# Performance work log

Measured on AMD Instinct MI355X. Metric: run time of the kernel, lower is better.

The kernel has to match this reference:

```python
import jax, jax.numpy as jnp
import numpy as np

B_, L_, D_ = 2, 1024, 512   # batch, seq_len, dim
H_ = 8                      # num_heads, head_dim = 64
Q_ = 64                     # chunk size for the chunked semi-separable scan


def setup_inputs() -> dict:
    key = jax.random.key(0)
    ks = jax.random.split(key, 7)
    s = 1.0 / np.sqrt(D_)   # torch nn.Linear default init bound
    x = jax.random.normal(ks[0], (B_, L_, D_), dtype=jnp.float32)
    W_A = jax.random.uniform(ks[1], (D_, D_), jnp.float32, -s, s)
    b_A = jax.random.uniform(ks[2], (D_,), jnp.float32, -s, s)
    W_B = jax.random.uniform(ks[3], (D_, D_), jnp.float32, -s, s)
    b_B = jax.random.uniform(ks[4], (D_,), jnp.float32, -s, s)
    W_C = jax.random.uniform(ks[5], (D_, D_), jnp.float32, -s, s)
    b_C = jax.random.uniform(ks[6], (D_,), jnp.float32, -s, s)
    return {"x": x, "W_A": W_A, "b_A": b_A, "W_B": W_B, "b_B": b_B,
            "W_C": W_C, "b_C": b_C}


def _semi_separable_T(x, W_A, b_A, W_B, b_B, W_C, b_C):
    """T_ij = sum_d C_{i,d} * (prod_{k=j+1}^{i-1} A_{k,d}) * B_{j,d}, j <= i.

    Computed in log space with Mamba2-style chunking: all exponent
    differences are <= 0, so exp() underflows to 0 (the true limit)
    instead of producing inf/nan as a naive cumprod-quotient would.
    """
    B, L, D = x.shape
    H = H_
    Dh = D // H
    Q = Q_
    nc = L // Q
    NEG = -jnp.inf

    A = jax.nn.sigmoid(x @ W_A.T + b_A)    # [B,L,D], values in (0,1)
    Bf = x @ W_B.T + b_B
    C = x @ W_C.T + b_C

    def heads(t):
        return t.reshape(B, L, H, Dh).transpose(0, 2, 1, 3)  # [B,H,L,Dh]

    A, Bf, C = heads(A), heads(Bf), heads(C)

    S = jnp.cumsum(jnp.log(A), axis=2)                       # S[k] = sum_{0..k} log A
    Sm1 = jnp.concatenate([jnp.zeros_like(S[:, :, :1]), S[:, :, :-1]], axis=2)
    # prod_{k=j+1}^{i-1} A_k = exp(Sm1[i] - S[j])  for i >= j+1 (==1 at i=j+1)

    def chunk(t):
        return t.reshape(B, H, nc, Q, Dh)

    Sc, Sm1c, Bc, Cc = chunk(S), chunk(Sm1), chunk(Bf), chunk(C)

    qi = jnp.arange(Q)[:, None]
    ki = jnp.arange(Q)[None, :]
    lower = (qi > ki)[None, None, None, :, :, None]
    diag = (qi == ki)[None, None, None, :, :, None]

    # ---- diagonal blocks (within-chunk, strictly lower + diagonal) ----
    diff = Sm1c[:, :, :, :, None, :] - Sc[:, :, :, None, :, :]  # [B,H,nc,Q,Q,Dh], <=0 where q>k
    dec = jnp.where(lower, diff, jnp.where(diag, 0.0, NEG))     # q==k -> prod=1
    Tdiag = jnp.einsum('bhmqd,bhmqkd,bhmkd->bhmqk', Cc, jnp.exp(dec), Bc)

    # ---- cross blocks (chunk m queries vs chunk n<m keys) ----
    E = Sc[:, :, :, -1, :]                                      # S at last index of each chunk
    Eprev = jnp.concatenate([jnp.zeros_like(E[:, :, :1]), E[:, :, :-1]], axis=2)
    qf = Cc * jnp.exp(Sm1c - Eprev[:, :, :, None, :])           # exponent <= 0
    kf = Bc * jnp.exp(E[:, :, :, None, :] - Sc)                 # exponent <= 0
    mi = jnp.arange(nc)[:, None]
    ni = jnp.arange(nc)[None, :]
    cross_mask = (ni < mi)[None, None, :, :, None]
    Dcross = jnp.exp(jnp.where(cross_mask,
                               Eprev[:, :, :, None, :] - E[:, :, None, :, :],
                               NEG))                            # [B,H,nc,nc,Dh]
    T = jnp.einsum('bhmqd,bhmnd,bhnkd->bhmqnk', qf, Dcross, kf)

    idx = jnp.arange(nc)
    T = T.at[:, :, idx, :, idx, :].set(jnp.moveaxis(Tdiag, 2, 0))
    return T.reshape(B, H, L, L)


def reference(x, W_A, b_A, W_B, b_B, W_C, b_C):
    return _semi_separable_T(x, W_A, b_A, W_B, b_B, W_C, b_C)
```

## Files before the change

### kernel.cpp

```cpp
#include <hip/hip_runtime.h>
#include <math.h>

#define BB 2
#define LL 1024
#define DD 512
#define HH 8
#define DHD 64
#define QQ 64
#define NCC 16

typedef __attribute__((ext_vector_type(8))) short s8b;
typedef __attribute__((ext_vector_type(4))) float f4;

__device__ __forceinline__ void bf16split(float f, unsigned short& h, unsigned short& l) {
    unsigned u  = __float_as_uint(f);
    unsigned hb = (u + 0x7FFFu + ((u >> 16) & 1u)) & 0xFFFF0000u;
    float fh = __uint_as_float(hb);
    float fl = f - fh;
    unsigned ul = __float_as_uint(fl);
    unsigned lb = (ul + 0x7FFFu + ((ul >> 16) & 1u)) >> 16;
    h = (unsigned short)(hb >> 16);
    l = (unsigned short)lb;
}

__device__ __forceinline__ unsigned pk2(unsigned short a, unsigned short b) {
    return (unsigned)a | ((unsigned)b << 16);
}

__global__ __launch_bounds__(512) void gemm3_fused(
    const float* __restrict__ x,
    const float* __restrict__ Wa, const float* __restrict__ ba,
    const float* __restrict__ Wb, const float* __restrict__ bb,
    const float* __restrict__ Wc, const float* __restrict__ bc,
    float* __restrict__ logA, float* __restrict__ Bf, float* __restrict__ Cf,
    float* __restrict__ csum)
{
    __shared__ unsigned char lds[65536];
    __shared__ float csv[64];

    const int bm = blockIdx.x >> 3;
    const int bn = blockIdx.x & 7;
    const int m0 = bm << 6, o0 = bn << 6;
    const int t = threadIdx.x, wv = t >> 6, ln = t & 63;
    const int l15 = ln & 15, l4 = ln >> 4;
    const int wr = (wv >> 2) << 5;
    const int wc = (wv & 3) << 4;

    const int src_id = wv >> 1;
    const float* srcp =
        (src_id == 0) ? x + (size_t)m0 * DD :
        ((src_id == 1) ? Wa : (src_id == 2) ? Wb : Wc) + (size_t)o0 * DD;
    const int roff = ((wv & 1) << 5) + (ln >> 1);
    const int ksh  = (ln & 1) << 4;
    const int swz  = (roff >> 1) & 3;
    const int sA   = ((ksh >> 3) + 0) ^ swz;
    const int sB   = ((ksh >> 3) + 1) ^ swz;
    const size_t srow = (size_t)roff * DD + ksh;
    const int hiBase = (src_id * 2) * 4096 + roff * 64;

    f4 acc[3][2] = {};

    auto STAGE = [&](int buf, int kt) {
        const float* p = srcp + srow + kt;
        const float4 f0 = *(const float4*)(p + 0);
        const float4 f1 = *(const float4*)(p + 4);
        const float4 f2 = *(const float4*)(p + 8);
        const float4 f3 = *(const float4*)(p + 12);
        const float v[16] = {f0.x,f0.y,f0.z,f0.w, f1.x,f1.y,f1.z,f1.w,
                             f2.x,f2.y,f2.z,f2.w, f3.x,f3.y,f3.z,f3.w};
        unsigned short h[16], l[16];
        #pragma unroll
        for (int i = 0; i < 16; ++i) bf16split(v[i], h[i], l[i]);
        unsigned char* bh = lds + buf * 32768 + hiBase;
        unsigned char* bl = bh + 4096;
        *(uint4*)(bh + sA * 16) = make_uint4(pk2(h[0],h[1]),  pk2(h[2],h[3]),
                                             pk2(h[4],h[5]),  pk2(h[6],h[7]));
        *(uint4*)(bh + sB * 16) = make_uint4(pk2(h[8],h[9]),  pk2(h[10],h[11]),
                                             pk2(h[12],h[13]),pk2(h[14],h[15]));
        *(uint4*)(bl + sA * 16) = make_uint4(pk2(l[0],l[1]),  pk2(l[2],l[3]),
                                             pk2(l[4],l[5]),  pk2(l[6],l[7]));
        *(uint4*)(bl + sB * 16) = make_uint4(pk2(l[8],l[9]),  pk2(l[10],l[11]),
                                             pk2(l[12],l[13]),pk2(l[14],l[15]));
    };

    auto ldso = [&](int row, int kg) {
        return row * 64 + ((kg ^ ((row >> 1) & 3)) << 4);
    };

    auto COMPUTE = [&](int buf) {
        const unsigned char* base = lds + buf * 32768;
        const s8b ah0 = *(const s8b*)(base + 0*4096 + ldso(wr      + l15, l4));
        const s8b ah1 = *(const s8b*)(base + 0*4096 + ldso(wr + 16 + l15, l4));
        const s8b al0 = *(const s8b*)(base + 1*4096 + ldso(wr      + l15, l4));
        const s8b al1 = *(const s8b*)(base + 1*4096 + ldso(wr + 16 + l15, l4));
        #pragma unroll
        for (int s = 0; s < 3; ++s) {
            const s8b bh = *(const s8b*)(base + (2 + 2*s)*4096 + ldso(wc + l15, l4));
            const s8b bl = *(const s8b*)(base + (3 + 2*s)*4096 + ldso(wc + l15, l4));
            acc[s][0] = __builtin_amdgcn_mfma_f32_16x16x32_bf16(ah0, bh, acc[s][0], 0, 0, 0);
            acc[s][1] = __builtin_amdgcn_mfma_f32_16x16x32_bf16(ah1, bh, acc[s][1], 0, 0, 0);
            acc[s][0] = __builtin_amdgcn_mfma_f32_16x16x32_bf16(ah0, bl, acc[s][0], 0, 0, 0);
            acc[s][1] = __builtin_amdgcn_mfma_f32_16x16x32_bf16(ah1, bl, acc[s][1], 0, 0, 0);
            acc[s][0] = __builtin_amdgcn_mfma_f32_16x16x32_bf16(al0, bh, acc[s][0], 0, 0, 0);
            acc[s][1] = __builtin_amdgcn_mfma_f32_16x16x32_bf16(al1, bh, acc[s][1], 0, 0, 0);
        }
    };

    STAGE(0, 0);
    __syncthreads();
    int cur = 0;
    for (int it = 0; it < 16; ++it) {
        if (it < 15) STAGE(cur ^ 1, (it + 1) * 32);
        COMPUTE(cur);
        __syncthreads();
        cur ^= 1;
    }

    const int col = o0 + wc + l15;
    const float bva = ba[col], bvb = bb[col], bvc = bc[col];
    float asum = 0.f;
    #pragma unroll
    for (int ms = 0; ms < 2; ++ms) {
        const int row0 = m0 + wr + ms * 16 + l4 * 4;
        #pragma unroll
        for (int r = 0; r < 4; ++r) {
            const size_t o = (size_t)(row0 + r) * DD + col;
            float va = acc[0][ms][r] + bva;
            va = fminf(va, 0.f) - log1pf(__expf(-fabsf(va)));
            logA[o] = va;
            asum += va;
            Bf[o] = acc[1][ms][r] + bvb;
            Cf[o] = acc[2][ms][r] + bvc;
        }
    }

    asum += __shfl_xor(asum, 16);
    asum += __shfl_xor(asum, 32);
    if (wv < 4 && l4 == 0) csv[wc + l15] = asum;
    __syncthreads();
    if (wv >= 4 && l4 == 0) {
        const int blkc = (((bm >> 4) * 8 + bn) << 4) + (bm & 15);
        csum[(size_t)blkc * DHD + wc + l15] = csv[wc + l15] + asum;
    }
}

__global__ __launch_bounds__(256) void scan_diag(
    const float* __restrict__ logA, const float* __restrict__ Bf,
    const float* __restrict__ Cf, const float* __restrict__ csum,
    float* __restrict__ qf, float* __restrict__ kf,
    float* __restrict__ coff, float* __restrict__ out)
{
    __shared__ float part[4][DHD];
    __shared__ float smA[DHD][65];
    __shared__ float smB[DHD][65];
    __shared__ float smC[DHD][65];

    const int blk = blockIdx.x;
    const int bh = blk >> 4, c = blk & 15;
    const int b = bh >> 3, h = bh & 7;
    const int t = threadIdx.x;
    const int d = t & 63, w = t >> 6;

    const size_t gbase = (size_t)(b * LL + c * QQ + w * 16) * DD + h * DHD + d;
    float lar[16];
    float ps = 0.f;
    #pragma unroll
    for (int i = 0; i < 16; ++i) {
        lar[i] = logA[gbase + (size_t)i * DD];
        ps += lar[i];
    }
    part[w][d] = ps;
    __syncthreads();

    const size_t cs0 = ((size_t)bh << 4) * DHD + d;
    float off = 0.f;
    for (int cc = 0; cc < c; ++cc) off += csum[cs0 + (size_t)cc * DHD];
    const float tot = part[0][d] + part[1][d] + part[2][d] + part[3][d];
    if (t < DHD) {
        coff[((size_t)bh * 17 + c) * DHD + t] = off;
        if (c == NCC - 1) coff[((size_t)bh * 17 + 16) * DHD + t] = off + tot;
    }

    float run = 0.f;
    for (int ww = 0; ww < 4; ++ww) if (ww < w) run += part[ww][d];

    const size_t hbase = ((size_t)bh * LL + c * QQ + w * 16) * DHD + d;
    #pragma unroll
    for (int i = 0; i < 16; ++i) {
        const size_t gi = gbase + (size_t)i * DD;
        const float cv = Cf[gi];
        const float bv = Bf[gi];
        qf[hbase + (size_t)i * DHD] = cv * __expf(run);
        run += lar[i];
        const int rloc = w * 16 + i;
        smC[d][rloc] = run;
        smA[d][rloc] = cv;
        smB[d][rloc] = bv;
        kf[hbase + (size_t)i * DHD] = bv * __expf(tot - run);
    }
    __syncthreads();

    const int q0 = ((t >> 4) & 15) << 2;
    const int k0 = (t & 15) << 2;

    float acc[4][4] = {};
    if (q0 + 3 >= k0) {
        #pragma unroll 2
        for (int dd = 0; dd < DHD; ++dd) {
            const float4 cq = *(const float4*)&smA[dd][q0];
            const float4 bk = *(const float4*)&smB[dd][k0];
            const float4 sk = *(const float4*)&smC[dd][k0];
            const float cqa[4] = {cq.x, cq.y, cq.z, cq.w};
            const float bka[4] = {bk.x, bk.y, bk.z, bk.w};
            const float ska[4] = {sk.x, sk.y, sk.z, sk.w};
            float s1a[4];
            #pragma unroll
            for (int i = 0; i < 4; ++i) {
                const int qi = q0 + i;
                s1a[i] = (qi == 0) ? 0.f : smC[dd][qi - 1];
            }
            #pragma unroll
            for (int i = 0; i < 4; ++i) {
                #pragma unroll
                for (int j = 0; j < 4; ++j) {
                    const int qi = q0 + i, kj = k0 + j;
                    const float wgt = (qi > kj) ? __expf(s1a[i] - ska[j])
                                                : ((qi == kj) ? 1.f : 0.f);
                    acc[i][j] += cqa[i] * wgt * bka[j];
                }
            }
        }
    }
    const size_t outrow0 = ((size_t)bh * LL + (size_t)c * QQ) * LL + (size_t)c * QQ;
    #pragma unroll
    for (int i = 0; i < 4; ++i)
        *(float4*)&out[outrow0 + (size_t)(q0 + i) * LL + k0] =
            make_float4(acc[i][0], acc[i][1], acc[i][2], acc[i][3]);

    for (int z = blk; z < BB * HH * 120; z += 256) {
        const int zbh = z / 120;
        const int idx = z - zbh * 120;
        int a = (int)((1.0f + sqrtf(1.0f + 8.0f * (float)idx)) * 0.5f);
        if (a * (a - 1) / 2 > idx) --a;
        else if ((a + 1) * a / 2 <= idx) ++a;
        const int zm = idx - a * (a - 1) / 2;
        const int zn = a;
        const size_t zb = ((size_t)zbh * LL + (size_t)zm * QQ) * LL + (size_t)zn * QQ;
        const float4 zz = make_float4(0.f, 0.f, 0.f, 0.f);
        #pragma unroll
        for (int r = 0; r < 4; ++r) {
            const int fi = t + (r << 8);
            const int row = fi >> 4;
            const int col = (fi & 15) << 2;
            *(float4*)&out[zb + (size_t)row * LL + col] = zz;
        }
    }
}

__global__ __launch_bounds__(256) void band_row(
    const float* __restrict__ qf, const float* __restrict__ kf,
    const float* __restrict__ coff, float* __restrict__ out)
{
    __shared__ unsigned char lds[49152];
    unsigned char* const l_qh = lds;
    unsigned char* const l_ql = lds + 8192;

    const int raw  = blockIdx.x;
    const int xcd  = raw & 7;
    const int kk   = raw >> 3;
    const int bh   = ((kk & 1) << 3) | xcd;
    const int rem  = kk >> 1;
    const int m    = rem >> 2;
    const int q4   = rem & 3;
    const int n0   = q4 << 2;

    const int t  = threadIdx.x;
    const int wv = t >> 6;
    const int ln = t & 63;
    const int l15 = ln & 15;
    const int l4  = ln >> 4;
    const int wr = (wv >> 1) << 5;
    const int wc = (wv & 1) << 5;

    const int srow = t >> 2;
    const int skc  = (t & 3) << 4;
    const int slot0 = skc >> 3;

    const size_t cb = (size_t)bh * 17 * DHD;
    const size_t outbase = ((size_t)bh * LL + (size_t)m * QQ) * LL;

    const int ne = (m < n0 + 4) ? m : (n0 + 4);
    if (n0 >= ne) return;

    float cm[16];
    #pragma unroll
    for (int g = 0; g < 4; ++g) {
        const float4 a = *(const float4*)&coff[cb + (size_t)m * DHD + skc + g * 4];
        cm[g*4+0]=a.x; cm[g*4+1]=a.y; cm[g*4+2]=a.z; cm[g*4+3]=a.w;
    }

    {
        const size_t qb = ((size_t)bh * LL + (size_t)m * QQ + srow) * DHD + skc;
        float v[16];
        #pragma unroll
        for (int g = 0; g < 4; ++g) {
            const float4 x4 = *(const float4*)&qf[qb + g * 4];
            v[g*4+0]=x4.x; v[g*4+1]=x4.y; v[g*4+2]=x4.z; v[g*4+3]=x4.w;
        }
        unsigned short h[16], l[16];
        #pragma unroll
        for (int i = 0; i < 16; ++i) bf16split(v[i], h[i], l[i]);
        *(uint4*)(l_qh + slot0*1024 + srow*16) =
            make_uint4(pk2(h[0],h[1]), pk2(h[2],h[3]), pk2(h[4],h[5]), pk2(h[6],h[7]));
        *(uint4*)(l_qh + (slot0+1)*1024 + srow*16) =
            make_uint4(pk2(h[8],h[9]), pk2(h[10],h[11]), pk2(h[12],h[13]), pk2(h[14],h[15]));
        *(uint4*)(l_ql + slot0*1024 + srow*16) =
            make_uint4(pk2(l[0],l[1]), pk2(l[2],l[3]), pk2(l[4],l[5]), pk2(l[6],l[7]));
        *(uint4*)(l_ql + (slot0+1)*1024 + srow*16) =
            make_uint4(pk2(l[8],l[9]), pk2(l[10],l[11]), pk2(l[12],l[13]), pk2(l[14],l[15]));
    }

    auto LOAD_K = [&](int n, float* vk, float* vc) {
        const size_t kb = ((size_t)bh * LL + (size_t)n * QQ + srow) * DHD + skc;
        #pragma unroll
        for (int g = 0; g < 4; ++g) {
            const float4 x4 = *(const float4*)&kf[kb + g * 4];
            vk[g*4+0]=x4.x; vk[g*4+1]=x4.y; vk[g*4+2]=x4.z; vk[g*4+3]=x4.w;
            const float4 c4 = *(const float4*)&coff[cb + (size_t)(n + 1) * DHD + skc + g * 4];
            vc[g*4+0]=c4.x; vc[g*4+1]=c4.y; vc[g*4+2]=c4.z; vc[g*4+3]=c4.w;
        }
    };

    auto WRITE_K = [&](int buf, const float* vk, const float* vc) {
        unsigned char* const kh_b = lds + 16384 + buf * 16384;
        unsigned char* const kl_b = kh_b + 8192;
        float v[16];
        #pragma unroll
        for (int i = 0; i < 16; ++i)
            v[i] = vk[i] * __expf(cm[i] - vc[i]);
        unsigned short h[16], l[16];
        #pragma unroll
        for (int i = 0; i < 16; ++i) bf16split(v[i], h[i], l[i]);
        *(uint4*)(kh_b + slot0*1024 + srow*16) =
            make_uint4(pk2(h[0],h[1]), pk2(h[2],h[3]), pk2(h[4],h[5]), pk2(h[6],h[7]));
        *(uint4*)(kh_b + (slot0+1)*1024 + srow*16) =
            make_uint4(pk2(h[8],h[9]), pk2(h[10],h[11]), pk2(h[12],h[13]), pk2(h[14],h[15]));
        *(uint4*)(kl_b + slot0*1024 + srow*16) =
            make_uint4(pk2(l[0],l[1]), pk2(l[2],l[3]), pk2(l[4],l[5]), pk2(l[6],l[7]));
        *(uint4*)(kl_b + (slot0+1)*1024 + srow*16) =
            make_uint4(pk2(l[8],l[9]), pk2(l[10],l[11]), pk2(l[12],l[13]), pk2(l[14],l[15]));
    };

    {
        float pk0[16], pc0[16];
        LOAD_K(n0, pk0, pc0);
        WRITE_K(0, pk0, pc0);
    }
    __syncthreads();

    int cur = 0;
    for (int n = n0; n < ne; ++n) {
        float nk[16], nc[16];
        const bool pre = (n + 1 < ne);
        if (pre) LOAD_K(n + 1, nk, nc);

        const unsigned char* const kh_b = lds + 16384 + cur * 16384;
        const unsigned char* const kl_b = kh_b + 8192;

        f4 acc[2][2] = {};
        #pragma unroll
        for (int ks = 0; ks < 2; ++ks) {
            const int ka = (ks * 4 + l4) * 1024;
            const s8b kh0 = *(const s8b*)(kh_b + ka + (wr      + l15) * 16);
            const s8b kh1 = *(const s8b*)(kh_b + ka + (wr + 16 + l15) * 16);
            const s8b kl0 = *(const s8b*)(kl_b + ka + (wr      + l15) * 16);
            const s8b kl1 = *(const s8b*)(kl_b + ka + (wr + 16 + l15) * 16);
            const s8b qh0 = *(const s8b*)(l_qh + ka + (wc      + l15) * 16);
            const s8b qh1 = *(const s8b*)(l_qh + ka + (wc + 16 + l15) * 16);
            const s8b ql0 = *(const s8b*)(l_ql + ka + (wc      + l15) * 16);
            const s8b ql1 = *(const s8b*)(l_ql + ka + (wc + 16 + l15) * 16);

            acc[0][0] = __builtin_amdgcn_mfma_f32_16x16x32_bf16(kh0, qh0, acc[0][0], 0, 0, 0);
            acc[0][1] = __builtin_amdgcn_mfma_f32_16x16x32_bf16(kh0, qh1, acc[0][1], 0, 0, 0);
            acc[1][0] = __builtin_amdgcn_mfma_f32_16x16x32_bf16(kh1, qh0, acc[1][0], 0, 0, 0);
            acc[1][1] = __builtin_amdgcn_mfma_f32_16x16x32_bf16(kh1, qh1, acc[1][1], 0, 0, 0);
            acc[0][0] = __builtin_amdgcn_mfma_f32_16x16x32_bf16(kh0, ql0, acc[0][0], 0, 0, 0);
            acc[0][1] = __builtin_amdgcn_mfma_f32_16x16x32_bf16(kh0, ql1, acc[0][1], 0, 0, 0);
            acc[1][0] = __builtin_amdgcn_mfma_f32_16x16x32_bf16(kh1, ql0, acc[1][0], 0, 0, 0);
            acc[1][1] = __builtin_amdgcn_mfma_f32_16x16x32_bf16(kh1, ql1, acc[1][1], 0, 0, 0);
            acc[0][0] = __builtin_amdgcn_mfma_f32_16x16x32_bf16(kl0, qh0, acc[0][0], 0, 0, 0);
            acc[0][1] = __builtin_amdgcn_mfma_f32_16x16x32_bf16(kl0, qh1, acc[0][1], 0, 0, 0);
            acc[1][0] = __builtin_amdgcn_mfma_f32_16x16x32_bf16(kl1, qh0, acc[1][0], 0, 0, 0);
            acc[1][1] = __builtin_amdgcn_mfma_f32_16x16x32_bf16(kl1, qh1, acc[1][1], 0, 0, 0);
        }

        #pragma unroll
        for (int ms = 0; ms < 2; ++ms) {
            #pragma unroll
            for (int ns = 0; ns < 2; ++ns) {
                const int q  = wc + ns * 16 + l15;
                const int k0 = wr + ms * 16 + l4 * 4;
                *(float4*)&out[outbase + (size_t)q * LL + (size_t)n * QQ + k0] =
                    make_float4(acc[ms][ns][0], acc[ms][ns][1], acc[ms][ns][2], acc[ms][ns][3]);
            }
        }

        if (pre) WRITE_K(cur ^ 1, nk, nc);

        __syncthreads();
        cur ^= 1;
    }
}

extern "C" void kernel_launch(void* const* d_in, const int* in_sizes, int n_in,
                              void* d_out, int out_size, void* d_ws, size_t ws_size,
                              hipStream_t stream) {
    const float* x  = (const float*)d_in[0];
    const float* Wa = (const float*)d_in[1];
    const float* ba = (const float*)d_in[2];
    const float* Wb = (const float*)d_in[3];
    const float* bb = (const float*)d_in[4];
    const float* Wc = (const float*)d_in[5];
    const float* bc = (const float*)d_in[6];
    float* out = (float*)d_out;
    float* ws  = (float*)d_ws;

    const size_t NBLD = (size_t)BB * LL * DD;
    float* logA = ws;
    float* Bf   = ws + 1 * NBLD;
    float* Cf   = ws + 2 * NBLD;
    float* qf   = ws + 4 * NBLD;
    float* kf   = ws + 5 * NBLD;
    float* coff = ws + 6 * NBLD;
    float* csum = coff + (size_t)BB * HH * 17 * DHD;

    gemm3_fused<<<256, 512, 0, stream>>>(x, Wa, ba, Wb, bb, Wc, bc, logA, Bf, Cf, csum);
    scan_diag<<<BB * HH * NCC, 256, 0, stream>>>(logA, Bf, Cf, csum, qf, kf, coff, out);
    band_row<<<BB * HH * NCC * 4, 256, 0, stream>>>(qf, kf, coff, out);
}
```

Baseline: 74.35 us.

## Pre-split weights to bf16 hi/lo and stage them via global_load_lds

Adds a kernel that converts the three weight matrices into bf16 hi/lo arrays once per call. The GEMM then loads these pre-split weights straight into LDS with global_load_lds and only splits the x tile in registers. The aim is to stop each of the 32 row blocks from redundantly converting the same weight tiles, and to cut the VGPR and ALU work in the staging loop. The cost is an extra kernel launch plus a write and re-read of 3 MB of converted weights, and the global-to-LDS loads now have to line up with the swizzled layout.

Result: no change. 75.19 us (+1.1%).

```diff
diff --git a/kernel.cpp b/kernel.cpp
--- a/kernel.cpp
+++ b/kernel.cpp
@@ -11,6 +11,12 @@
 
 typedef __attribute__((ext_vector_type(8))) short s8b;
 typedef __attribute__((ext_vector_type(4))) float f4;
+
+__device__ __forceinline__ void gld16(const void* g, void* l) {
+    __builtin_amdgcn_global_load_lds(
+        (const __attribute__((address_space(1))) unsigned int*)g,
+        (__attribute__((address_space(3))) unsigned int*)l, 16, 0, 0);
+}
 
 __device__ __forceinline__ void bf16split(float f, unsigned short& h, unsigned short& l) {
     unsigned u  = __float_as_uint(f);
@@ -27,11 +33,29 @@
     return (unsigned)a | ((unsigned)b << 16);
 }
 
+__global__ __launch_bounds__(256) void convert_w(
+    const float* __restrict__ Wa, const float* __restrict__ Wb,
+    const float* __restrict__ Wc,
+    unsigned short* __restrict__ wh, unsigned short* __restrict__ wl)
+{
+    const int g = blockIdx.x * 256 + threadIdx.x;
+    const size_t j = (size_t)g * 4;
+    const int wsel = (int)(j >> 18);
+    const size_t r = j & 262143;
+    const float* src = (wsel == 0 ? Wa : (wsel == 1 ? Wb : Wc)) + r;
+    const float4 v = *(const float4*)src;
+    const float f[4] = {v.x, v.y, v.z, v.w};
+    unsigned short h[4], l[4];
+    #pragma unroll
+    for (int i = 0; i < 4; ++i) bf16split(f[i], h[i], l[i]);
+    *(uint2*)&wh[j] = make_uint2(pk2(h[0], h[1]), pk2(h[2], h[3]));
+    *(uint2*)&wl[j] = make_uint2(pk2(l[0], l[1]), pk2(l[2], l[3]));
+}
+
 __global__ __launch_bounds__(512) void gemm3_fused(
     const float* __restrict__ x,
-    const float* __restrict__ Wa, const float* __restrict__ ba,
-    const float* __restrict__ Wb, const float* __restrict__ bb,
-    const float* __restrict__ Wc, const float* __restrict__ bc,
+    const unsigned short* __restrict__ wh, const unsigned short* __restrict__ wl,
+    const float* __restrict__ ba, const float* __restrict__ bb, const float* __restrict__ bc,
     float* __restrict__ logA, float* __restrict__ Bf, float* __restrict__ Cf,
     float* __restrict__ csum)
 {
@@ -46,41 +70,41 @@
     const int wr = (wv >> 2) << 5;
     const int wc = (wv & 3) << 4;
 
-    const int src_id = wv >> 1;
-    const float* srcp =
-        (src_id == 0) ? x + (size_t)m0 * DD :
-        ((src_id == 1) ? Wa : (src_id == 2) ? Wb : Wc) + (size_t)o0 * DD;
-    const int roff = ((wv & 1) << 5) + (ln >> 1);
-    const int ksh  = (ln & 1) << 4;
-    const int swz  = (roff >> 1) & 3;
-    const int sA   = ((ksh >> 3) + 0) ^ swz;
-    const int sB   = ((ksh >> 3) + 1) ^ swz;
-    const size_t srow = (size_t)roff * DD + ksh;
-    const int hiBase = (src_id * 2) * 4096 + roff * 64;
+    const int xrow = t >> 3;
+    const int xfq  = t & 7;
+    const int xslot = (xfq >> 1) ^ ((xrow >> 1) & 3);
+    const int xbyte = xrow * 64 + (xslot << 4) + ((xfq & 1) << 3);
+    const float* xp = x + (size_t)(m0 + xrow) * DD + xfq * 4;
+
+    size_t wofs[3];
+    int    wdst[3];
+    const unsigned short* wsrc[3];
+    #pragma unroll
+    for (int j = 0; j < 3; ++j) {
+        const int c = wv + j * 8;
+        const int a = c >> 2;
+        const int s = c & 3;
+        const int row16 = (s << 4) + (ln >> 2);
+        const int kg_src = (ln & 3) ^ ((row16 >> 1) & 3);
+        wsrc[j] = ((a & 1) ? wl : wh) + (size_t)(a >> 1) * 262144;
+        wofs[j] = (size_t)(o0 + row16) * DD + kg_src * 8;
+        wdst[j] = (2 + a) * 4096 + s * 1024;
+    }
 
     f4 acc[3][2] = {};
 
     auto STAGE = [&](int buf, int kt) {
-        const float* p = srcp + srow + kt;
-        const float4 f0 = *(const float4*)(p + 0);
-        const float4 f1 = *(const float4*)(p + 4);
-        const float4 f2 = *(const float4*)(p + 8);
-        const float4 f3 = *(const float4*)(p + 12);
-        const float v[16] = {f0.x,f0.y,f0.z,f0.w, f1.x,f1.y,f1.z,f1.w,
-                             f2.x,f2.y,f2.z,f2.w, f3.x,f3.y,f3.z,f3.w};
-        unsigned short h[16], l[16];
-        #pragma unroll
-        for (int i = 0; i < 16; ++i) bf16split(v[i], h[i], l[i]);
-        unsigned char* bh = lds + buf * 32768 + hiBase;
-        unsigned char* bl = bh + 4096;
-        *(uint4*)(bh + sA * 16) = make_uint4(pk2(h[0],h[1]),  pk2(h[2],h[3]),
-                                             pk2(h[4],h[5]),  pk2(h[6],h[7]));
-        *(uint4*)(bh + sB * 16) = make_uint4(pk2(h[8],h[9]),  pk2(h[10],h[11]),
-                                             pk2(h[12],h[13]),pk2(h[14],h[15]));
-        *(uint4*)(bl + sA * 16) = make_uint4(pk2(l[0],l[1]),  pk2(l[2],l[3]),
-                                             pk2(l[4],l[5]),  pk2(l[6],l[7]));
-        *(uint4*)(bl + sB * 16) = make_uint4(pk2(l[8],l[9]),  pk2(l[10],l[11]),
-                                             pk2(l[12],l[13]),pk2(l[14],l[15]));
+        #pragma unroll
+        for (int j = 0; j < 3; ++j)
+            gld16(wsrc[j] + wofs[j] + kt, lds + buf * 32768 + wdst[j]);
+        const float4 xv = *(const float4*)(xp + kt);
+        unsigned short h[4], l[4];
+        bf16split(xv.x, h[0], l[0]);
+        bf16split(xv.y, h[1], l[1]);
+        bf16split(xv.z, h[2], l[2]);
+        bf16split(xv.w, h[3], l[3]);
+        *(uint2*)(lds + buf * 32768 + 0 * 4096 + xbyte) = make_uint2(pk2(h[0], h[1]), pk2(h[2], h[3]));
+        *(uint2*)(lds + buf * 32768 + 1 * 4096 + xbyte) = make_uint2(pk2(l[0], l[1]), pk2(l[2], l[3]));
     };
 
     auto ldso = [&](int row, int kg) {
@@ -434,7 +458,11 @@
     float* coff = ws + 6 * NBLD;
     float* csum = coff + (size_t)BB * HH * 17 * DHD;
 
-    gemm3_fused<<<256, 512, 0, stream>>>(x, Wa, ba, Wb, bb, Wc, bc, logA, Bf, Cf, csum);
+    unsigned short* wh = (unsigned short*)(ws + 3 * NBLD);
+    unsigned short* wl = wh + 786432;
+
+    convert_w<<<768, 256, 0, stream>>>(Wa, Wb, Wc, wh, wl);
+    gemm3_fused<<<256, 512, 0, stream>>>(x, wh, wl, ba, bb, bc, logA, Bf, Cf, csum);
     scan_diag<<<BB * HH * NCC, 256, 0, stream>>>(logA, Bf, Cf, csum, qf, kf, coff, out);
     band_row<<<BB * HH * NCC * 4, 256, 0, stream>>>(qf, kf, coff, out);
 }
```
